# Optimization experiments

Measured on AMD Instinct MI355X. Metric: run time of the kernel, lower is better.

The kernel has to match this reference:

```python
import jax, jax.numpy as jnp
import numpy as np

B, S, F = 4, 4096, 1024
H, DK, R = 16, 64, 32  # n_head, d_k, low_rank; n_attn = H*DK = 1024


def _l2norm(x, eps=1e-12):
    # torch.nn.functional.normalize(p=2, dim=-1)
    n = jnp.sqrt(jnp.sum(x * x, axis=-1, keepdims=True))
    return x / jnp.maximum(n, eps)


def setup_inputs() -> dict:
    key = jax.random.key(0)
    ks = jax.random.split(key, 16)
    s = 0.02
    inp = {
        "query": jax.random.normal(ks[0], (B, S, F), jnp.float32),
        "key": jax.random.normal(ks[1], (B, S, F), jnp.float32),
        "value": jax.random.normal(ks[2], (B, S, F), jnp.float32),
        "p_layer": 1,
        # linear_q / linear_k (linear_v unused in p_layer branch but kept for fidelity)
        "Wq": jax.random.normal(ks[3], (H * DK, F), jnp.float32) * s,
        "bq": jnp.zeros((H * DK,), jnp.float32),
        "Wk": jax.random.normal(ks[4], (H * DK, F), jnp.float32) * s,
        "bk": jnp.zeros((H * DK,), jnp.float32),
        "Wv": jax.random.normal(ks[5], (H * DK, F), jnp.float32) * s,
        "bv": jnp.zeros((H * DK,), jnp.float32),
        # low-rank projections (orthogonal-init stand-ins)
        "We": jax.random.normal(ks[6], (H, DK, R), jnp.float32) * s,
        "Wr": jax.random.normal(ks[7], (H, DK, R), jnp.float32) * s,
        "Lam": jax.random.uniform(ks[8], (H, R), jnp.float32),
        # concate_weight: Linear(2R -> DK)
        "Wc": jax.random.normal(ks[9], (DK, 2 * R), jnp.float32) * s,
        "bc": jnp.zeros((DK,), jnp.float32),
        # linear_out: Linear(H*DK -> F)
        "Wo": jax.random.normal(ks[10], (F, H * DK), jnp.float32) * s,
        "bo": jnp.zeros((F,), jnp.float32),
    }
    return inp


def reference(query, key, value, Wq, bq, Wk, bk, Wv, bv, We, Wr, Lam, Wc, bc, Wo, bo, p_layer):
    n_batch, seq_len, _ = query.shape
    # projections -> (B, H, S, DK)
    q = (query @ Wq.T + bq).reshape(n_batch, seq_len, H, DK).transpose(0, 2, 1, 3)
    k = (key @ Wk.T + bk).reshape(n_batch, seq_len, H, DK).transpose(0, 2, 1, 3)
    if p_layer:  # static Python int
        normal = jnp.arange(1, seq_len + 1, dtype=q.dtype)[None, None, :, None]
        q = jnp.cumsum(q, axis=2) / normal  # causal running average
        k = jnp.cumsum(k, axis=2) / normal
        q = _l2norm(q)
        k = _l2norm(k)
        escore = jnp.einsum('bhnd,hde->bhne', q, We)  # (B,H,S,R)
        rscore = jnp.einsum('bhnd,hde->bhne', k, Wr)
        scores = jnp.concatenate((escore, rscore), axis=-1)  # (B,H,S,2R)
        x = scores @ Wc.T + bc  # (B,H,S,DK)
        x = x.transpose(0, 2, 1, 3).reshape(n_batch, seq_len, H * DK)
    else:
        v = (value @ Wv.T + bv).reshape(n_batch, seq_len, H, DK).transpose(0, 2, 1, 3)
        att = jax.nn.softmax(jnp.einsum('bhqd,bhkd->bhqk', q, k) / jnp.sqrt(jnp.asarray(DK, q.dtype)), axis=-1)
        x = jnp.einsum('bhqk,bhkd->bhqd', att, v).transpose(0, 2, 1, 3).reshape(n_batch, seq_len, H * DK)
    return x @ Wo.T + bo
```

## Files before the change

### kernel.cpp

```cpp
#include <hip/hip_runtime.h>

typedef __bf16 bf16x8 __attribute__((ext_vector_type(8)));
typedef float floatx4 __attribute__((ext_vector_type(4)));

__device__ __forceinline__ unsigned short f2bf(float x) {
  union { float f; unsigned u; } v; v.f = x;
  unsigned u = v.u;
  unsigned r = (u + 0x7FFFu + ((u >> 16) & 1u)) >> 16;
  return (unsigned short)r;
}
__device__ __forceinline__ float bf2f(unsigned short x) {
  union { unsigned u; float f; } v; v.u = ((unsigned)x) << 16;
  return v.f;
}
__device__ __forceinline__ float fast_rcp(float x) {
#if defined(__has_builtin) && __has_builtin(__builtin_amdgcn_rcpf)
  return __builtin_amdgcn_rcpf(x);
#else
  return 1.0f / x;
#endif
}
__device__ __forceinline__ float fast_rsq(float x) {
#if defined(__has_builtin) && __has_builtin(__builtin_amdgcn_rsqf)
  return __builtin_amdgcn_rsqf(x);
#else
  return 1.0f / sqrtf(x);
#endif
}

__device__ __forceinline__ void stage16(const unsigned short* __restrict__ g,
                                        unsigned short* s, int lane) {
#if defined(__has_builtin) && __has_builtin(__builtin_amdgcn_global_load_lds)
  __builtin_amdgcn_global_load_lds((const __attribute__((address_space(1))) void*)g,
                                   (__attribute__((address_space(3))) void*)s,
                                   16, 0, 0);
#else
  *(uint4*)(s + (size_t)lane * 8) = *(const uint4*)g;
#endif
}

__global__ void cvt_bf16(const float* __restrict__ in, unsigned short* __restrict__ out, int n4) {
  int i = blockIdx.x * 256 + threadIdx.x;
  if (i >= n4) return;
  const float4 v = ((const float4*)in)[i];
  ushort4 o;
  o.x = f2bf(v.x); o.y = f2bf(v.y); o.z = f2bf(v.z); o.w = f2bf(v.w);
  ((ushort4*)out)[i] = o;
}

#define LDSE (256 * 64)

#define RD_A(b, mh) {                                                          \
  _Pragma("unroll") for (int ii = 0; ii < 4; ++ii) {                           \
    _Pragma("unroll") for (int s = 0; s < 2; ++s) {                            \
      af[ii][s] = *(const bf16x8*)(rA + (b) * LDSE +                           \
                                   ((mh) * 128 + ii * 16) * 64 +               \
                                   (((s << 2) | quad) ^ key) * 8);             \
    } } }

#define RD_B(b, nh, dst) {                                                     \
  _Pragma("unroll") for (int jj = 0; jj < 2; ++jj) {                           \
    _Pragma("unroll") for (int s = 0; s < 2; ++s) {                            \
      dst[jj][s] = *(const bf16x8*)(rB + (b) * LDSE +                          \
                                    ((nh) * 128 + jj * 16) * 64 +              \
                                    (((s << 2) | quad) ^ key) * 8);            \
    } } }

#define STAGE_A(b, mh, t) {                                                    \
  stage16(gA + (size_t)((mh) * 128) * K + (size_t)(t) * 64,                    \
          sAw + (b) * LDSE + ((mh) * 128) * 64, lane);                         \
  stage16(gA + (size_t)((mh) * 128 + 8) * K + (size_t)(t) * 64,                \
          sAw + (b) * LDSE + ((mh) * 128 + 8) * 64, lane); }

#define STAGE_B(b, nh, t) {                                                    \
  stage16(gB + (size_t)((nh) * 128) * K + (size_t)(t) * 64,                    \
          sBw + (b) * LDSE + ((nh) * 128) * 64, lane);                         \
  stage16(gB + (size_t)((nh) * 128 + 8) * K + (size_t)(t) * 64,                \
          sBw + (b) * LDSE + ((nh) * 128 + 8) * 64, lane); }

#define MIDSYNC()                                                              \
  __builtin_amdgcn_s_barrier();                                                \
  asm volatile("s_waitcnt lgkmcnt(0)" ::: "memory");

#define MFMA_PH(mh, nh, bfx) {                                                 \
  __builtin_amdgcn_s_setprio(1);                                               \
  _Pragma("unroll") for (int s = 0; s < 2; ++s) {                              \
    _Pragma("unroll") for (int ii = 0; ii < 4; ++ii) {                         \
      _Pragma("unroll") for (int jj = 0; jj < 2; ++jj) {                       \
        acc[mh][nh][ii][jj] = __builtin_amdgcn_mfma_f32_16x16x32_bf16(         \
            af[ii][s], bfx[jj][s], acc[mh][nh][ii][jj], 0, 0, 0);              \
      } } }                                                                    \
  __builtin_amdgcn_s_setprio(0); }

#define TILE(b, t, S1, S234, MORE) {                                           \
                                                               \
  RD_A(b, 0); RD_B(b, 0, bf0);                                                 \
  if (S1) { STAGE_A((b) ^ 1, 1, (t) + 1); }                                    \
  MIDSYNC(); MFMA_PH(0, 0, bf0); __builtin_amdgcn_s_barrier();                 \
                                                               \
  RD_B(b, 1, bf1);                                                             \
  if (S234) { STAGE_A(b, 0, (t) + 2); }                                        \
  MIDSYNC(); MFMA_PH(0, 1, bf1); __builtin_amdgcn_s_barrier();                 \
                                                               \
  RD_A(b, 1);                                                                  \
  if (S234) { STAGE_B(b, 0, (t) + 2); }                                        \
  MIDSYNC(); MFMA_PH(1, 1, bf1); __builtin_amdgcn_s_barrier();                 \
                                                               \
  if (S234) { STAGE_B(b, 1, (t) + 2); }                                        \
  if (MORE) { asm volatile("s_waitcnt vmcnt(6)" ::: "memory"); }               \
  else      { asm volatile("s_waitcnt vmcnt(0)" ::: "memory"); }               \
  MIDSYNC(); MFMA_PH(1, 0, bf0); __builtin_amdgcn_s_barrier(); }

template <int OUT_BF16>
__global__ __launch_bounds__(512, 2) void gemm8p(const unsigned short* __restrict__ A,
                                                 const unsigned short* __restrict__ B,
                                                 const float* __restrict__ bias,
                                                 void* __restrict__ Cv,
                                                 int M, int N, int K) {
  __shared__ unsigned short As[2 * 256 * 64];
  __shared__ unsigned short Bs[2 * 256 * 64];
  const int tid = threadIdx.x;
  const int w = tid >> 6;
  const int lane = tid & 63;

  const int NT = N >> 8;
  const int id = blockIdx.x;
  const int x = id & 7;
  const int g = id >> 3;
  const int nt_ = g % NT;
  const int mt = x + 8 * (g / NT);
  const int bm = mt * 256, bn = nt_ * 256;

  const int row16 = lane & 15, quad = lane >> 4, key = lane & 7;
  const int l8 = lane >> 3, lk = lane & 7;
  const int swz = (lk ^ l8) * 8;

  const unsigned short* gA = A + (size_t)(bm + 16 * w + l8) * K + swz;
  const unsigned short* gB = B + (size_t)(bn + 16 * w + l8) * K + swz;
  unsigned short* sAw = As + (16 * w) * 64;
  unsigned short* sBw = Bs + (16 * w) * 64;

  const unsigned short* rA = As + ((w >> 2) * 64 + row16) * 64;
  const unsigned short* rB = Bs + ((w & 3) * 32 + row16) * 64;

  floatx4 acc[2][2][4][2] = {};
  bf16x8 af[4][2], bf0[2][2], bf1[2][2];

  STAGE_A(0, 0, 0); STAGE_B(0, 0, 0); STAGE_B(0, 1, 0); STAGE_A(0, 1, 0);
  STAGE_A(1, 0, 1); STAGE_B(1, 0, 1); STAGE_B(1, 1, 1);
  asm volatile("s_waitcnt vmcnt(6)" ::: "memory");
  __builtin_amdgcn_s_barrier();

  const int npair = K >> 7;
  for (int it = 0; it < npair; ++it) {
    const int t0 = it * 2;
    const bool more = (it + 1 < npair);
    TILE(0, t0, true, more, more);
    TILE(1, t0 + 1, more, more, more);
  }

#pragma unroll
  for (int nh = 0; nh < 2; ++nh)
#pragma unroll
    for (int jj = 0; jj < 2; ++jj) {
      const int gcol = bn + nh * 128 + (w & 3) * 32 + jj * 16 + row16;
      const float bb = bias ? bias[gcol] : 0.0f;
#pragma unroll
      for (int mh = 0; mh < 2; ++mh)
#pragma unroll
        for (int ii = 0; ii < 4; ++ii) {
          const int grow = bm + mh * 128 + (w >> 2) * 64 + ii * 16 + quad * 4;
#pragma unroll
          for (int r = 0; r < 4; ++r) {
            float v = acc[mh][nh][ii][jj][r] + bb;
            if (OUT_BF16)
              ((unsigned short*)Cv)[(size_t)(grow + r) * N + gcol] = f2bf(v);
            else
              ((float*)Cv)[(size_t)(grow + r) * N + gcol] = v;
          }
        }
    }
}

__global__ void scan_partial(const unsigned short* __restrict__ proj, float* __restrict__ partial) {
  const int t = blockIdx.x, chunk = blockIdx.y, b = blockIdx.z;
  const int c4 = threadIdx.x * 4;
  const unsigned short* p =
      proj + ((size_t)t * 4 + b) * 4096 * 1024 + (size_t)chunk * 64 * 1024 + c4;
  float4 s = {0.f, 0.f, 0.f, 0.f};
  for (int i = 0; i < 64; i++) {
    const ushort4 v = *(const ushort4*)(p + (size_t)i * 1024);
    s.x += bf2f(v.x); s.y += bf2f(v.y); s.z += bf2f(v.z); s.w += bf2f(v.w);
  }
  *(float4*)(partial + ((size_t)(t * 4 + b) * 64 + chunk) * 1024 + c4) = s;
}

__global__ void scan_apply(const unsigned short* __restrict__ proj,
                           const float* __restrict__ partial,
                           unsigned short* __restrict__ qkn) {
  const int t = blockIdx.x, chunk = blockIdx.y, b = blockIdx.z;
  const int c4 = threadIdx.x * 4;
  const float* pp = partial + (size_t)(t * 4 + b) * 64 * 1024 + c4;
  float4 run = {0.f, 0.f, 0.f, 0.f};
  for (int j = 0; j < chunk; j++) {
    const float4 v = *(const float4*)(pp + (size_t)j * 1024);
    run.x += v.x; run.y += v.y; run.z += v.z; run.w += v.w;
  }
  const unsigned short* p =
      proj + ((size_t)t * 4 + b) * 4096 * 1024 + (size_t)chunk * 64 * 1024 + c4;
  unsigned short* o = qkn + (size_t)b * 4096 * 2048 + (size_t)chunk * 64 * 2048 + t * 1024 + c4;
  for (int i = 0; i < 64; i++) {
    const ushort4 v = *(const ushort4*)(p + (size_t)i * 1024);
    run.x += bf2f(v.x); run.y += bf2f(v.y); run.z += bf2f(v.z); run.w += bf2f(v.w);
    const int s = chunk * 64 + i;
    const float inv = fast_rcp((float)(s + 1));
    const float a0 = run.x * inv, a1 = run.y * inv, a2 = run.z * inv, a3 = run.w * inv;
    float sq = a0 * a0 + a1 * a1 + a2 * a2 + a3 * a3;
    sq += __shfl_xor(sq, 8);
    sq += __shfl_xor(sq, 4);
    sq += __shfl_xor(sq, 2);
    sq += __shfl_xor(sq, 1);
    const float sc = fast_rsq(fmaxf(sq, 1e-24f));
    ushort4 ov;
    ov.x = f2bf(a0 * sc); ov.y = f2bf(a1 * sc); ov.z = f2bf(a2 * sc); ov.w = f2bf(a3 * sc);
    *(ushort4*)(o + (size_t)i * 2048) = ov;
  }
}

__global__ void make_A(const float* __restrict__ We, const float* __restrict__ Wr,
                       const float* __restrict__ Wc, float* __restrict__ Asm) {
  const int t = blockIdx.x >> 4, h = blockIdx.x & 15;
  const float* W = (t ? Wr : We) + (size_t)h * 64 * 32;
  for (int e = threadIdx.x; e < 4096; e += 256) {
    const int d = e >> 6, dk = e & 63;
    float s = 0.f;
    for (int r = 0; r < 32; r++) s += W[d * 32 + r] * Wc[dk * 64 + t * 32 + r];
    Asm[(size_t)blockIdx.x * 4096 + e] = s;
  }
}

__global__ __launch_bounds__(256) void make_G(const float* __restrict__ Asm,
                                              const float* __restrict__ Wo,
                                              unsigned short* __restrict__ Gt) {
  __shared__ float At[64 * 65];
  __shared__ float WoSh[64 * 64];
  const int th = blockIdx.x, t = th >> 4, h = th & 15;
  const int f0 = blockIdx.y * 64;
  const int tid = threadIdx.x;
  for (int e = tid; e < 4096; e += 256) {
    const int d = e >> 6, dk = e & 63;
    At[dk * 65 + d] = Asm[(size_t)th * 4096 + e];
  }
  for (int e = tid; e < 4096; e += 256) {
    const int fl = e >> 6, dk = e & 63;
    WoSh[e] = Wo[(size_t)(f0 + fl) * 1024 + h * 64 + dk];
  }
  __syncthreads();
  const int d = tid & 63;
  const int fsub = tid >> 6;
#pragma unroll 4
  for (int it = 0; it < 16; ++it) {
    const int fl = it * 4 + fsub;
    float s = 0.f;
#pragma unroll
    for (int dk4 = 0; dk4 < 16; ++dk4) {
      const float4 wv = *(const float4*)&WoSh[fl * 64 + dk4 * 4];
      s += At[(dk4 * 4 + 0) * 65 + d] * wv.x + At[(dk4 * 4 + 1) * 65 + d] * wv.y +
           At[(dk4 * 4 + 2) * 65 + d] * wv.z + At[(dk4 * 4 + 3) * 65 + d] * wv.w;
    }
    Gt[(size_t)(f0 + fl) * 2048 + t * 1024 + h * 64 + d] = f2bf(s);
  }
}

__global__ void make_c0(const float* __restrict__ bc, const float* __restrict__ bo,
                        const float* __restrict__ Wo, float* __restrict__ c0) {
  const int f = blockIdx.x * 4 + (threadIdx.x >> 6);
  const int lane = threadIdx.x & 63;
  const float bcl = bc[lane];
  float s = 0.f;
  for (int j = lane; j < 1024; j += 64) s += bcl * Wo[(size_t)f * 1024 + j];
#pragma unroll
  for (int off = 32; off; off >>= 1) s += __shfl_xor(s, off);
  if (lane == 0) c0[f] = s + bo[f];
}

extern "C" void kernel_launch(void* const* d_in, const int* in_sizes, int n_in,
                              void* d_out, int out_size, void* d_ws, size_t ws_size,
                              hipStream_t stream) {
  const float* query = (const float*)d_in[0];
  const float* key_  = (const float*)d_in[1];
  const float* Wq = (const float*)d_in[4];
  const float* bq = (const float*)d_in[5];
  const float* Wk = (const float*)d_in[6];
  const float* bk = (const float*)d_in[7];
  const float* We = (const float*)d_in[10];
  const float* Wr = (const float*)d_in[11];
  const float* Wc = (const float*)d_in[13];
  const float* bc = (const float*)d_in[14];
  const float* Wo = (const float*)d_in[15];
  const float* bo = (const float*)d_in[16];

  char* ws = (char*)d_ws;
  unsigned short* qkbf = (unsigned short*)ws;
  unsigned short* Wbf  = (unsigned short*)(ws + 67108864);
  unsigned short* Gt   = (unsigned short*)(ws + 71303168);
  float* partial       = (float*)(ws + 71303168);
  float* Asm           = (float*)(ws + 75497472);
  float* c0            = (float*)(ws + 76021760);

  unsigned short* proj = (unsigned short*)d_out;

  cvt_bf16<<<16384, 256, 0, stream>>>(query, qkbf, 4194304);
  cvt_bf16<<<16384, 256, 0, stream>>>(key_, qkbf + 16777216, 4194304);
  cvt_bf16<<<1024, 256, 0, stream>>>(Wq, Wbf, 262144);
  cvt_bf16<<<1024, 256, 0, stream>>>(Wk, Wbf + 1048576, 262144);

  gemm8p<1><<<256, 512, 0, stream>>>(qkbf, Wbf, bq, proj, 16384, 1024, 1024);
  gemm8p<1><<<256, 512, 0, stream>>>(qkbf + 16777216, Wbf + 1048576, bk,
                                     proj + 16777216, 16384, 1024, 1024);

  scan_partial<<<dim3(2, 64, 4), 256, 0, stream>>>(proj, partial);
  scan_apply<<<dim3(2, 64, 4), 256, 0, stream>>>(proj, partial, qkbf);

  make_A<<<32, 256, 0, stream>>>(We, Wr, Wc, Asm);
  make_G<<<dim3(32, 16), 256, 0, stream>>>(Asm, Wo, Gt);
  make_c0<<<256, 256, 0, stream>>>(bc, bo, Wo, c0);

  gemm8p<0><<<256, 512, 0, stream>>>(qkbf, Gt, c0, (float*)d_out, 16384, 1024, 2048);
}
```

Measured before the change: 459.4 us.

## Restructure GEMM pipeline waits and halve scan chunk length

Reworks the GEMM main loop so LDS reads and global stages are issued before the MFMA phase. It drops the lgkmcnt(0) mid-phase barrier, uses finer vmcnt waits, and peels the final tile pair into an explicit drain epilogue. Separately, the causal-scan kernels use 128 chunks of 32 rows instead of 64 of 64, which doubles the grid to improve occupancy at the cost of a longer serial prefix over partials. The partial buffer doubles to 4 MiB and shares the region used for Gt, which is written later. It is also adjacent to Asm, so it risks touching that boundary.

```diff
diff --git a/kernel.cpp b/kernel.cpp
--- a/kernel.cpp
+++ b/kernel.cpp
@@ -50,6 +50,10 @@
 
 #define LDSE (256 * 64)
 
+#define VMW_(n) asm volatile("s_waitcnt vmcnt(" #n ")" ::: "memory")
+#define VMW(n) VMW_(n)
+#define BAR() __builtin_amdgcn_s_barrier()
+
 #define RD_A(b, mh) {                                                          \
   _Pragma("unroll") for (int ii = 0; ii < 4; ++ii) {                           \
     _Pragma("unroll") for (int s = 0; s < 2; ++s) {                            \
@@ -77,10 +81,6 @@
           sBw + (b) * LDSE + ((nh) * 128) * 64, lane);                         \
   stage16(gB + (size_t)((nh) * 128 + 8) * K + (size_t)(t) * 64,                \
           sBw + (b) * LDSE + ((nh) * 128 + 8) * 64, lane); }
-
-#define MIDSYNC()                                                              \
-  __builtin_amdgcn_s_barrier();                                                \
-  asm volatile("s_waitcnt lgkmcnt(0)" ::: "memory");
 
 #define MFMA_PH(mh, nh, bfx) {                                                 \
   __builtin_amdgcn_s_setprio(1);                                               \
@@ -92,24 +92,15 @@
       } } }                                                                    \
   __builtin_amdgcn_s_setprio(0); }
 
-#define TILE(b, t, S1, S234, MORE) {                                           \
-                                                               \
-  RD_A(b, 0); RD_B(b, 0, bf0);                                                 \
-  if (S1) { STAGE_A((b) ^ 1, 1, (t) + 1); }                                    \
-  MIDSYNC(); MFMA_PH(0, 0, bf0); __builtin_amdgcn_s_barrier();                 \
-                                                               \
-  RD_B(b, 1, bf1);                                                             \
-  if (S234) { STAGE_A(b, 0, (t) + 2); }                                        \
-  MIDSYNC(); MFMA_PH(0, 1, bf1); __builtin_amdgcn_s_barrier();                 \
-                                                               \
-  RD_A(b, 1);                                                                  \
-  if (S234) { STAGE_B(b, 0, (t) + 2); }                                        \
-  MIDSYNC(); MFMA_PH(1, 1, bf1); __builtin_amdgcn_s_barrier();                 \
-                                                               \
-  if (S234) { STAGE_B(b, 1, (t) + 2); }                                        \
-  if (MORE) { asm volatile("s_waitcnt vmcnt(6)" ::: "memory"); }               \
-  else      { asm volatile("s_waitcnt vmcnt(0)" ::: "memory"); }               \
-  MIDSYNC(); MFMA_PH(1, 0, bf0); __builtin_amdgcn_s_barrier(); }
+#define TILE_ST(b, t) {                                                        \
+  RD_B(b, 0, bf0); RD_A(b, 0); STAGE_A((b) ^ 1, 1, (t) + 1);                   \
+  MFMA_PH(0, 0, bf0); VMW(10); BAR();                                          \
+  RD_B(b, 1, bf1); STAGE_A(b, 0, (t) + 2);                                     \
+  MFMA_PH(0, 1, bf1); VMW(10); BAR();                                          \
+  RD_A(b, 1); STAGE_B(b, 0, (t) + 2);                                          \
+  MFMA_PH(1, 1, bf1); BAR();                                                   \
+  STAGE_B(b, 1, (t) + 2);                                                      \
+  MFMA_PH(1, 0, bf0); VMW(10); BAR(); }
 
 template <int OUT_BF16>
 __global__ __launch_bounds__(512, 2) void gemm8p(const unsigned short* __restrict__ A,
@@ -148,15 +139,32 @@
 
   STAGE_A(0, 0, 0); STAGE_B(0, 0, 0); STAGE_B(0, 1, 0); STAGE_A(0, 1, 0);
   STAGE_A(1, 0, 1); STAGE_B(1, 0, 1); STAGE_B(1, 1, 1);
-  asm volatile("s_waitcnt vmcnt(6)" ::: "memory");
-  __builtin_amdgcn_s_barrier();
+  VMW(10);
+  BAR();
 
   const int npair = K >> 7;
-  for (int it = 0; it < npair; ++it) {
+  for (int it = 0; it < npair - 1; ++it) {
     const int t0 = it * 2;
-    const bool more = (it + 1 < npair);
-    TILE(0, t0, true, more, more);
-    TILE(1, t0 + 1, more, more, more);
+    TILE_ST(0, t0);
+    TILE_ST(1, t0 + 1);
+  }
+
+  {
+    const int T = 2 * npair - 2;
+    RD_B(0, 0, bf0); RD_A(0, 0); STAGE_A(1, 1, T + 1);
+    MFMA_PH(0, 0, bf0); VMW(10); BAR();
+    RD_B(0, 1, bf1);
+    MFMA_PH(0, 1, bf1); VMW(8); BAR();
+    RD_A(0, 1);
+    MFMA_PH(1, 1, bf1); BAR();
+    MFMA_PH(1, 0, bf0); VMW(4); BAR();
+    RD_B(1, 0, bf0); RD_A(1, 0);
+    MFMA_PH(0, 0, bf0); VMW(2); BAR();
+    RD_B(1, 1, bf1);
+    MFMA_PH(0, 1, bf1); VMW(0); BAR();
+    RD_A(1, 1);
+    MFMA_PH(1, 1, bf1); BAR();
+    MFMA_PH(1, 0, bf0);
   }
 
 #pragma unroll
@@ -186,13 +194,13 @@
   const int t = blockIdx.x, chunk = blockIdx.y, b = blockIdx.z;
   const int c4 = threadIdx.x * 4;
   const unsigned short* p =
-      proj + ((size_t)t * 4 + b) * 4096 * 1024 + (size_t)chunk * 64 * 1024 + c4;
+      proj + ((size_t)t * 4 + b) * 4096 * 1024 + (size_t)chunk * 32 * 1024 + c4;
   float4 s = {0.f, 0.f, 0.f, 0.f};
-  for (int i = 0; i < 64; i++) {
+  for (int i = 0; i < 32; i++) {
     const ushort4 v = *(const ushort4*)(p + (size_t)i * 1024);
     s.x += bf2f(v.x); s.y += bf2f(v.y); s.z += bf2f(v.z); s.w += bf2f(v.w);
   }
-  *(float4*)(partial + ((size_t)(t * 4 + b) * 64 + chunk) * 1024 + c4) = s;
+  *(float4*)(partial + ((size_t)(t * 4 + b) * 128 + chunk) * 1024 + c4) = s;
 }
 
 __global__ void scan_apply(const unsigned short* __restrict__ proj,
@@ -200,19 +208,19 @@
                            unsigned short* __restrict__ qkn) {
   const int t = blockIdx.x, chunk = blockIdx.y, b = blockIdx.z;
   const int c4 = threadIdx.x * 4;
-  const float* pp = partial + (size_t)(t * 4 + b) * 64 * 1024 + c4;
+  const float* pp = partial + (size_t)(t * 4 + b) * 128 * 1024 + c4;
   float4 run = {0.f, 0.f, 0.f, 0.f};
   for (int j = 0; j < chunk; j++) {
     const float4 v = *(const float4*)(pp + (size_t)j * 1024);
     run.x += v.x; run.y += v.y; run.z += v.z; run.w += v.w;
   }
   const unsigned short* p =
-      proj + ((size_t)t * 4 + b) * 4096 * 1024 + (size_t)chunk * 64 * 1024 + c4;
-  unsigned short* o = qkn + (size_t)b * 4096 * 2048 + (size_t)chunk * 64 * 2048 + t * 1024 + c4;
-  for (int i = 0; i < 64; i++) {
+      proj + ((size_t)t * 4 + b) * 4096 * 1024 + (size_t)chunk * 32 * 1024 + c4;
+  unsigned short* o = qkn + (size_t)b * 4096 * 2048 + (size_t)chunk * 32 * 2048 + t * 1024 + c4;
+  for (int i = 0; i < 32; i++) {
     const ushort4 v = *(const ushort4*)(p + (size_t)i * 1024);
     run.x += bf2f(v.x); run.y += bf2f(v.y); run.z += bf2f(v.z); run.w += bf2f(v.w);
-    const int s = chunk * 64 + i;
+    const int s = chunk * 32 + i;
     const float inv = fast_rcp((float)(s + 1));
     const float a0 = run.x * inv, a1 = run.y * inv, a2 = run.z * inv, a3 = run.w * inv;
     float sq = a0 * a0 + a1 * a1 + a2 * a2 + a3 * a3;
@@ -319,8 +327,8 @@
   gemm8p<1><<<256, 512, 0, stream>>>(qkbf + 16777216, Wbf + 1048576, bk,
                                      proj + 16777216, 16384, 1024, 1024);
 
-  scan_partial<<<dim3(2, 64, 4), 256, 0, stream>>>(proj, partial);
-  scan_apply<<<dim3(2, 64, 4), 256, 0, stream>>>(proj, partial, qkbf);
+  scan_partial<<<dim3(2, 128, 4), 256, 0, stream>>>(proj, partial);
+  scan_apply<<<dim3(2, 128, 4), 256, 0, stream>>>(proj, partial, qkbf);
 
   make_A<<<32, 256, 0, stream>>>(We, Wr, Wc, Asm);
   make_G<<<dim3(32, 16), 256, 0, stream>>>(Asm, Wo, Gt);
```

After: 461.3 us. No clear change (+0.4%).
